# Kernel tuning notes

Hardware: AMD Instinct MI355X
Metric: run time of the kernel (lower is better)

Reference implementation:

```python
import jax, jax.numpy as jnp
import numpy as np


def setup_inputs() -> dict:
    key = jax.random.key(0)
    ks = jax.random.split(key, 4)
    B, T, I, H, O = 1024, 512, 64, 128, 10
    return {
        "x": jax.random.normal(ks[0], (B, T, I), dtype=jnp.float32),
        "W_hx": jax.random.normal(ks[1], (H, I), dtype=jnp.float32) * (6.0 / (H + I)) ** 0.5,
        "W_hh": jax.random.normal(ks[2], (H, H), dtype=jnp.float32) * (6.0 / (H + H)) ** 0.5,
        "b_hh": jnp.zeros((H,), dtype=jnp.float32),
        "W_ph": jax.random.normal(ks[3], (O, H), dtype=jnp.float32) * (6.0 / (O + H)) ** 0.5,
        "b_ph": jnp.zeros((O,), dtype=jnp.float32),
    }


def reference(x, W_hx, W_hh, b_hh, W_ph, b_ph):
    B, T, I = x.shape
    H = W_hh.shape[0]
    # Precompute input projections for all timesteps in one GEMM: [B,T,H]
    xproj = jnp.einsum("bti,hi->bth", x, W_hx)
    h0 = jnp.zeros((B, H), dtype=x.dtype)

    def step(h, xp_t):
        # xp_t: [B,H]; recurrent update h = tanh(W_hx x_t + W_hh h + b)
        h_new = jnp.tanh(xp_t + h @ W_hh.T + b_hh)
        return h_new, None

    # scan over time (leading axis): xproj transposed to [T,B,H]
    h_T, _ = jax.lax.scan(step, h0, jnp.swapaxes(xproj, 0, 1))
    return h_T @ W_ph.T + b_ph
```

## Files before the change

kernel.cpp:

```cpp
#include <hip/hip_runtime.h>
#include <math.h>


#define T_STEPS 512
#define I_DIM   64
#define H_DIM   128
#define O_DIM   10
#define BT      16
#define PITCH   136
#define XPITCH  18

typedef short  bf16x8 __attribute__((ext_vector_type(8)));
typedef float  f32x4  __attribute__((ext_vector_type(4)));

#define MFMA(A, Bi, C) __builtin_amdgcn_mfma_f32_16x16x32_bf16((A), __builtin_bit_cast(bf16x8, (Bi)), (C), 0, 0, 0)

static __device__ inline short f2bf(float f) {
    union { float f; unsigned u; } v; v.f = f;
    unsigned r = v.u + 0x7FFFu + ((v.u >> 16) & 1u);
    return (short)(r >> 16);
}
static __device__ inline int pk2(float a, float b) {
    unsigned ua = __builtin_bit_cast(unsigned, a);
    unsigned ub = __builtin_bit_cast(unsigned, b);
    return (int)(((ua + 0x8000u) >> 16) | ((ub + 0x8000u) & 0xFFFF0000u));
}
static __device__ inline float bf2f(short s) {
    union { unsigned u; float f; } v; v.u = ((unsigned)(unsigned short)s) << 16;
    return v.f;
}
static __device__ inline void lds_barrier() {
    asm volatile("s_waitcnt lgkmcnt(0)\n\ts_barrier" ::: "memory");
}
static __device__ inline int4 load_frag(const float* src) {
    short e[8];
    #pragma unroll
    for (int j = 0; j < 8; ++j) e[j] = f2bf(src[j]);
    int4 r;
    r.x = ((int)(unsigned short)e[0]) | ((int)(unsigned short)e[1] << 16);
    r.y = ((int)(unsigned short)e[2]) | ((int)(unsigned short)e[3] << 16);
    r.z = ((int)(unsigned short)e[4]) | ((int)(unsigned short)e[5] << 16);
    r.w = ((int)(unsigned short)e[6]) | ((int)(unsigned short)e[7] << 16);
    return r;
}

#define CONS_STEP(P)                                                            \
    {                                                                           \
        const short* hb = hbuf[P] + c * PITCH + q * 8;                          \
        bf16x8 Ah0 = *(const bf16x8*)(hb +  0);                                 \
        bf16x8 Ah1 = *(const bf16x8*)(hb + 32);                                 \
        bf16x8 Ah2 = *(const bf16x8*)(hb + 64);                                 \
        bf16x8 Ah3 = *(const bf16x8*)(hb + 96);                                 \
        f32x4 Ca0 = *(const f32x4*)&xpb[P][ n0      * XPITCH + 4 * q];          \
        f32x4 Ca1 = *(const f32x4*)&xpb[P][(n0 + 1) * XPITCH + 4 * q];          \
        f32x4 Cb0 = {0.f, 0.f, 0.f, 0.f};                                       \
        f32x4 Cb1 = {0.f, 0.f, 0.f, 0.f};                                       \
        Ca0 = MFMA(Ah0, Bw[0][0], Ca0); Ca1 = MFMA(Ah0, Bw[1][0], Ca1);         \
        Cb0 = MFMA(Ah1, Bw[0][1], Cb0); Cb1 = MFMA(Ah1, Bw[1][1], Cb1);         \
        Ca0 = MFMA(Ah2, Bw[0][2], Ca0); Ca1 = MFMA(Ah2, Bw[1][2], Ca1);         \
        Cb0 = MFMA(Ah3, Bw[0][3], Cb0); Cb1 = MFMA(Ah3, Bw[1][3], Cb1);         \
        const f32x4 C0 = Ca0 + Cb0;                                             \
        const f32x4 C1 = Ca1 + Cb1;                                             \
        short* hw = hbuf[1 - (P)];                                              \
        _Pragma("unroll")                                                       \
        for (int r = 0; r < 4; ++r) {                                           \
            const int m = q * 4 + r;                                            \
            const float z0 = C0[r], z1 = C1[r];                                 \
            const float t0 = z0 * z0, t1 = z1 * z1;                             \
            const float p0 = fmaf(fmaf(t0 + 378.f, t0, 17325.f), t0, 135135.f); \
            const float p1 = fmaf(fmaf(t1 + 378.f, t1, 17325.f), t1, 135135.f); \
            const float q0 = fmaf(fmaf(fmaf(28.f, t0, 3150.f), t0, 62370.f), t0, 135135.f); \
            const float q1 = fmaf(fmaf(fmaf(28.f, t1, 3150.f), t1, 62370.f), t1, 135135.f); \
            const float rr = __builtin_amdgcn_rcpf(q0 * q1);                    \
            const float h0 = __builtin_amdgcn_fmed3f(z0 * p0 * (rr * q1), -1.f, 1.f); \
            const float h1 = __builtin_amdgcn_fmed3f(z1 * p1 * (rr * q0), -1.f, 1.f); \
            *(int*)(hw + m * PITCH + n0) = pk2(h0, h1);                         \
        }                                                                       \
    }

#define PROD_STEP(P, XR, TN)                                                    \
    {                                                                           \
        int4 a0, a1;                                                            \
        a0.x = pk2(XR[0].x, XR[0].y); a0.y = pk2(XR[0].z, XR[0].w);             \
        a0.z = pk2(XR[1].x, XR[1].y); a0.w = pk2(XR[1].z, XR[1].w);             \
        a1.x = pk2(XR[2].x, XR[2].y); a1.y = pk2(XR[2].z, XR[2].w);             \
        a1.z = pk2(XR[3].x, XR[3].y); a1.w = pk2(XR[3].z, XR[3].w);             \
        const int tn = ((TN) < T_STEPS) ? (TN) : (T_STEPS - 1);                 \
        const float* pn = xrow + (size_t)tn * I_DIM;                            \
        XR[0] = *(const float4*)(pn +      q * 8);                              \
        XR[1] = *(const float4*)(pn +      q * 8 + 4);                          \
        XR[2] = *(const float4*)(pn + 32 + q * 8);                              \
        XR[3] = *(const float4*)(pn + 32 + q * 8 + 4);                          \
        bf16x8 Ax0 = __builtin_bit_cast(bf16x8, a0);                            \
        bf16x8 Ax1 = __builtin_bit_cast(bf16x8, a1);                            \
        f32x4 P0 = MFMA(Ax0, BX[0][0], biasv[0]);                               \
        P0 = MFMA(Ax1, BX[0][1], P0);                                           \
        f32x4 P1 = MFMA(Ax0, BX[1][0], biasv[1]);                               \
        P1 = MFMA(Ax1, BX[1][1], P1);                                           \
        *(f32x4*)&xpb[1 - (P)][ n0      * XPITCH + 4 * q] = P0;                 \
        *(f32x4*)&xpb[1 - (P)][(n0 + 1) * XPITCH + 4 * q] = P1;                 \
    }

__global__ __launch_bounds__(512, 2)
void rnn_mfma_kernel(
    const float* __restrict__ x,
    const float* __restrict__ W_hx,
    const float* __restrict__ W_hh,
    const float* __restrict__ b_hh,
    const float* __restrict__ W_ph,
    const float* __restrict__ b_ph,
    float* __restrict__ out)
{
    const int b0   = blockIdx.x * BT;
    const int tid  = threadIdx.x;
    const int wave = tid >> 6;
    const int lane = tid & 63;
    const int c    = lane & 15;
    const int q    = lane >> 4;
    const int w    = wave & 3;
    const int n0   = w * 32 + 2 * c;

    __shared__ __align__(16) short hbuf[2][BT * PITCH];
    __shared__ __align__(16) float xpb[2][H_DIM * XPITCH];

    for (int idx = tid; idx < BT * PITCH; idx += 512) hbuf[0][idx] = 0;

    if (wave < 4) {
        int4 Bw[2][4];
        #pragma unroll
        for (int nt = 0; nt < 2; ++nt)
            #pragma unroll
            for (int kt = 0; kt < 4; ++kt)
                Bw[nt][kt] = load_frag(W_hh + (n0 + nt) * H_DIM + kt * 32 + q * 8);
        #pragma unroll
        for (int nt = 0; nt < 2; ++nt)
            #pragma unroll
            for (int kt = 0; kt < 4; ++kt)
                asm volatile("" : "+v"(Bw[nt][kt].x), "+v"(Bw[nt][kt].y),
                                  "+v"(Bw[nt][kt].z), "+v"(Bw[nt][kt].w));
        __syncthreads();
        __builtin_amdgcn_s_setprio(1);
        #pragma unroll 1
        for (int t = 0; t < T_STEPS; t += 2) {
            CONS_STEP(0)
            lds_barrier();
            CONS_STEP(1)
            lds_barrier();
        }
        __builtin_amdgcn_s_setprio(0);
    } else {
        int4 BX[2][2];
        f32x4 biasv[2];
        #pragma unroll
        for (int nt = 0; nt < 2; ++nt) {
            #pragma unroll
            for (int kx = 0; kx < 2; ++kx)
                BX[nt][kx] = load_frag(W_hx + (n0 + nt) * I_DIM + kx * 32 + q * 8);
            const float bb = b_hh[n0 + nt];
            biasv[nt] = (f32x4){bb, bb, bb, bb};
        }
        #pragma unroll
        for (int nt = 0; nt < 2; ++nt)
            #pragma unroll
            for (int kx = 0; kx < 2; ++kx)
                asm volatile("" : "+v"(BX[nt][kx].x), "+v"(BX[nt][kx].y),
                                  "+v"(BX[nt][kx].z), "+v"(BX[nt][kx].w));

        const float* xrow = x + (size_t)(b0 + c) * T_STEPS * I_DIM;
        {
            float4 x0[4];
            x0[0] = *(const float4*)(xrow +      q * 8);
            x0[1] = *(const float4*)(xrow +      q * 8 + 4);
            x0[2] = *(const float4*)(xrow + 32 + q * 8);
            x0[3] = *(const float4*)(xrow + 32 + q * 8 + 4);
            int4 a0, a1;
            a0.x = pk2(x0[0].x, x0[0].y); a0.y = pk2(x0[0].z, x0[0].w);
            a0.z = pk2(x0[1].x, x0[1].y); a0.w = pk2(x0[1].z, x0[1].w);
            a1.x = pk2(x0[2].x, x0[2].y); a1.y = pk2(x0[2].z, x0[2].w);
            a1.z = pk2(x0[3].x, x0[3].y); a1.w = pk2(x0[3].z, x0[3].w);
            bf16x8 Ax0 = __builtin_bit_cast(bf16x8, a0);
            bf16x8 Ax1 = __builtin_bit_cast(bf16x8, a1);
            f32x4 P0 = MFMA(Ax0, BX[0][0], biasv[0]);
            P0 = MFMA(Ax1, BX[0][1], P0);
            f32x4 P1 = MFMA(Ax0, BX[1][0], biasv[1]);
            P1 = MFMA(Ax1, BX[1][1], P1);
            *(f32x4*)&xpb[0][ n0      * XPITCH + 4 * q] = P0;
            *(f32x4*)&xpb[0][(n0 + 1) * XPITCH + 4 * q] = P1;
        }
        float4 xrA[4], xrB[4];
        const float* p1 = xrow + I_DIM;
        xrA[0] = *(const float4*)(p1 +      q * 8);
        xrA[1] = *(const float4*)(p1 +      q * 8 + 4);
        xrA[2] = *(const float4*)(p1 + 32 + q * 8);
        xrA[3] = *(const float4*)(p1 + 32 + q * 8 + 4);
        const float* p2 = xrow + 2 * I_DIM;
        xrB[0] = *(const float4*)(p2 +      q * 8);
        xrB[1] = *(const float4*)(p2 +      q * 8 + 4);
        xrB[2] = *(const float4*)(p2 + 32 + q * 8);
        xrB[3] = *(const float4*)(p2 + 32 + q * 8 + 4);
        __syncthreads();
        #pragma unroll 1
        for (int t = 0; t < T_STEPS; t += 2) {
            PROD_STEP(0, xrA, t + 3)
            lds_barrier();
            PROD_STEP(1, xrB, t + 4)
            lds_barrier();
        }
    }

    if (tid < BT * O_DIM) {
        const int m = tid / O_DIM;
        const int o = tid % O_DIM;
        float acc = b_ph[o];
        #pragma unroll 4
        for (int k = 0; k < H_DIM; ++k)
            acc = fmaf(W_ph[o * H_DIM + k], bf2f(hbuf[0][m * PITCH + k]), acc);
        out[(size_t)(b0 + m) * O_DIM + o] = acc;
    }
}

extern "C" void kernel_launch(void* const* d_in, const int* in_sizes, int n_in,
                              void* d_out, int out_size, void* d_ws, size_t ws_size,
                              hipStream_t stream) {
    const float* x    = (const float*)d_in[0];
    const float* W_hx = (const float*)d_in[1];
    const float* W_hh = (const float*)d_in[2];
    const float* b_hh = (const float*)d_in[3];
    const float* W_ph = (const float*)d_in[4];
    const float* b_ph = (const float*)d_in[5];
    float* out = (float*)d_out;

    rnn_mfma_kernel<<<1024 / BT, 512, 0, stream>>>(x, W_hx, W_hh, b_hh, W_ph, b_ph, out);
}
```

Baseline: 467.0 us.

## Prefetch input projections a step ahead into registers via ring LDS buffer

The producer waves now run one step further ahead, writing input projections into a two-slot ring buffer laid out per consumer lane. The consumer waves load the next step's projection accumulators right after issuing their MFMAs rather than at the start of each step, which takes that LDS read off the recurrent critical path. The layout change from the padded per-column buffer to a [64][36] ring is also meant to give conflict-free contiguous f32x4 accesses. The cost is extra registers in the consumer and a deeper producer lead, which depends on the barrier ordering staying correct across the ring slots.

```diff
diff --git a/kernel.cpp b/kernel.cpp
--- a/kernel.cpp
+++ b/kernel.cpp
@@ -8,7 +8,6 @@
 #define O_DIM   10
 #define BT      16
 #define PITCH   136
-#define XPITCH  18
 
 typedef short  bf16x8 __attribute__((ext_vector_type(8)));
 typedef float  f32x4  __attribute__((ext_vector_type(4)));
@@ -44,21 +43,23 @@
     return r;
 }
 
-#define CONS_STEP(P)                                                            \
+#define CONS_STEP(P, S0, S1, N0, N1)                                            \
     {                                                                           \
         const short* hb = hbuf[P] + c * PITCH + q * 8;                          \
         bf16x8 Ah0 = *(const bf16x8*)(hb +  0);                                 \
         bf16x8 Ah1 = *(const bf16x8*)(hb + 32);                                 \
         bf16x8 Ah2 = *(const bf16x8*)(hb + 64);                                 \
         bf16x8 Ah3 = *(const bf16x8*)(hb + 96);                                 \
-        f32x4 Ca0 = *(const f32x4*)&xpb[P][ n0      * XPITCH + 4 * q];          \
-        f32x4 Ca1 = *(const f32x4*)&xpb[P][(n0 + 1) * XPITCH + 4 * q];          \
+        f32x4 Ca0 = S0, Ca1 = S1;                                               \
         f32x4 Cb0 = {0.f, 0.f, 0.f, 0.f};                                       \
         f32x4 Cb1 = {0.f, 0.f, 0.f, 0.f};                                       \
         Ca0 = MFMA(Ah0, Bw[0][0], Ca0); Ca1 = MFMA(Ah0, Bw[1][0], Ca1);         \
         Cb0 = MFMA(Ah1, Bw[0][1], Cb0); Cb1 = MFMA(Ah1, Bw[1][1], Cb1);         \
         Ca0 = MFMA(Ah2, Bw[0][2], Ca0); Ca1 = MFMA(Ah2, Bw[1][2], Ca1);         \
         Cb0 = MFMA(Ah3, Bw[0][3], Cb0); Cb1 = MFMA(Ah3, Bw[1][3], Cb1);         \
+                \
+        N0 = *(const f32x4*)&xpring[1 - (P)][cp][4 * q];                        \
+        N1 = *(const f32x4*)&xpring[1 - (P)][cp][16 + 4 * q];                   \
         const f32x4 C0 = Ca0 + Cb0;                                             \
         const f32x4 C1 = Ca1 + Cb1;                                             \
         short* hw = hbuf[1 - (P)];                                              \
@@ -97,8 +98,8 @@
         P0 = MFMA(Ax1, BX[0][1], P0);                                           \
         f32x4 P1 = MFMA(Ax0, BX[1][0], biasv[1]);                               \
         P1 = MFMA(Ax1, BX[1][1], P1);                                           \
-        *(f32x4*)&xpb[1 - (P)][ n0      * XPITCH + 4 * q] = P0;                 \
-        *(f32x4*)&xpb[1 - (P)][(n0 + 1) * XPITCH + 4 * q] = P1;                 \
+        *(f32x4*)&xpring[P][cp][4 * q]      = P0;                               \
+        *(f32x4*)&xpring[P][cp][16 + 4 * q] = P1;                               \
     }
 
 __global__ __launch_bounds__(512, 2)
@@ -119,9 +120,10 @@
     const int q    = lane >> 4;
     const int w    = wave & 3;
     const int n0   = w * 32 + 2 * c;
+    const int cp   = 16 * w + c;
 
     __shared__ __align__(16) short hbuf[2][BT * PITCH];
-    __shared__ __align__(16) float xpb[2][H_DIM * XPITCH];
+    __shared__ __align__(16) float xpring[2][64][36];
 
     for (int idx = tid; idx < BT * PITCH; idx += 512) hbuf[0][idx] = 0;
 
@@ -139,12 +141,15 @@
                 asm volatile("" : "+v"(Bw[nt][kt].x), "+v"(Bw[nt][kt].y),
                                   "+v"(Bw[nt][kt].z), "+v"(Bw[nt][kt].w));
         __syncthreads();
+        f32x4 SA0 = *(const f32x4*)&xpring[0][cp][4 * q];
+        f32x4 SA1 = *(const f32x4*)&xpring[0][cp][16 + 4 * q];
+        f32x4 SB0, SB1;
         __builtin_amdgcn_s_setprio(1);
         #pragma unroll 1
         for (int t = 0; t < T_STEPS; t += 2) {
-            CONS_STEP(0)
-            lds_barrier();
-            CONS_STEP(1)
+            CONS_STEP(0, SA0, SA1, SB0, SB1)
+            lds_barrier();
+            CONS_STEP(1, SB0, SB1, SA0, SA1)
             lds_barrier();
         }
         __builtin_amdgcn_s_setprio(0);
@@ -167,43 +172,45 @@
                                   "+v"(BX[nt][kx].z), "+v"(BX[nt][kx].w));
 
         const float* xrow = x + (size_t)(b0 + c) * T_STEPS * I_DIM;
-        {
-            float4 x0[4];
-            x0[0] = *(const float4*)(xrow +      q * 8);
-            x0[1] = *(const float4*)(xrow +      q * 8 + 4);
-            x0[2] = *(const float4*)(xrow + 32 + q * 8);
-            x0[3] = *(const float4*)(xrow + 32 + q * 8 + 4);
+        #pragma unroll
+        for (int s = 0; s < 2; ++s) {
+            const float* ps = xrow + (size_t)s * I_DIM;
+            float4 xv[4];
+            xv[0] = *(const float4*)(ps +      q * 8);
+            xv[1] = *(const float4*)(ps +      q * 8 + 4);
+            xv[2] = *(const float4*)(ps + 32 + q * 8);
+            xv[3] = *(const float4*)(ps + 32 + q * 8 + 4);
             int4 a0, a1;
-            a0.x = pk2(x0[0].x, x0[0].y); a0.y = pk2(x0[0].z, x0[0].w);
-            a0.z = pk2(x0[1].x, x0[1].y); a0.w = pk2(x0[1].z, x0[1].w);
-            a1.x = pk2(x0[2].x, x0[2].y); a1.y = pk2(x0[2].z, x0[2].w);
-            a1.z = pk2(x0[3].x, x0[3].y); a1.w = pk2(x0[3].z, x0[3].w);
+            a0.x = pk2(xv[0].x, xv[0].y); a0.y = pk2(xv[0].z, xv[0].w);
+            a0.z = pk2(xv[1].x, xv[1].y); a0.w = pk2(xv[1].z, xv[1].w);
+            a1.x = pk2(xv[2].x, xv[2].y); a1.y = pk2(xv[2].z, xv[2].w);
+            a1.z = pk2(xv[3].x, xv[3].y); a1.w = pk2(xv[3].z, xv[3].w);
             bf16x8 Ax0 = __builtin_bit_cast(bf16x8, a0);
             bf16x8 Ax1 = __builtin_bit_cast(bf16x8, a1);
             f32x4 P0 = MFMA(Ax0, BX[0][0], biasv[0]);
             P0 = MFMA(Ax1, BX[0][1], P0);
             f32x4 P1 = MFMA(Ax0, BX[1][0], biasv[1]);
             P1 = MFMA(Ax1, BX[1][1], P1);
-            *(f32x4*)&xpb[0][ n0      * XPITCH + 4 * q] = P0;
-            *(f32x4*)&xpb[0][(n0 + 1) * XPITCH + 4 * q] = P1;
+            *(f32x4*)&xpring[s][cp][4 * q]      = P0;
+            *(f32x4*)&xpring[s][cp][16 + 4 * q] = P1;
         }
         float4 xrA[4], xrB[4];
-        const float* p1 = xrow + I_DIM;
-        xrA[0] = *(const float4*)(p1 +      q * 8);
-        xrA[1] = *(const float4*)(p1 +      q * 8 + 4);
-        xrA[2] = *(const float4*)(p1 + 32 + q * 8);
-        xrA[3] = *(const float4*)(p1 + 32 + q * 8 + 4);
         const float* p2 = xrow + 2 * I_DIM;
-        xrB[0] = *(const float4*)(p2 +      q * 8);
-        xrB[1] = *(const float4*)(p2 +      q * 8 + 4);
-        xrB[2] = *(const float4*)(p2 + 32 + q * 8);
-        xrB[3] = *(const float4*)(p2 + 32 + q * 8 + 4);
+        xrA[0] = *(const float4*)(p2 +      q * 8);
+        xrA[1] = *(const float4*)(p2 +      q * 8 + 4);
+        xrA[2] = *(const float4*)(p2 + 32 + q * 8);
+        xrA[3] = *(const float4*)(p2 + 32 + q * 8 + 4);
+        const float* p3 = xrow + 3 * I_DIM;
+        xrB[0] = *(const float4*)(p3 +      q * 8);
+        xrB[1] = *(const float4*)(p3 +      q * 8 + 4);
+        xrB[2] = *(const float4*)(p3 + 32 + q * 8);
+        xrB[3] = *(const float4*)(p3 + 32 + q * 8 + 4);
         __syncthreads();
         #pragma unroll 1
         for (int t = 0; t < T_STEPS; t += 2) {
-            PROD_STEP(0, xrA, t + 3)
-            lds_barrier();
-            PROD_STEP(1, xrB, t + 4)
+            PROD_STEP(0, xrA, t + 4)
+            lds_barrier();
+            PROD_STEP(1, xrB, t + 5)
             lds_barrier();
         }
     }
```

Result: no change. 465.3 us (-0.4%).
